# Performance work log

Hardware: AMD Instinct MI355X
Metric: run time of the kernel (lower is better)

## Reference

```python
import jax, jax.numpy as jnp
import numpy as np

N_NODES = 10000
N_EDGES = 160000
MUL0, MUL1 = 32, 8            # multiplicities of 0e and 1o irreps
IN_DIM = MUL0 + 3 * MUL1      # 56
EDGE_FEAT = 64
HIDDEN = 64
# FullyConnectedTensorProduct paths (in x sh -> out):
# (0e,0e)->0e : 32*32=1024 ; (0e,1o)->1o : 32*8=256
# (1o,0e)->1o : 8*8=64     ; (1o,1o)->0e : 8*32=256
W_NUMEL = 1024 + 256 + 64 + 256  # 1600
PATH_NORM = 1.0 / np.sqrt(MUL0 + MUL1)  # 'element' path normalization (fan_in=40)
CG_110 = 1.0 / np.sqrt(3.0)             # normalized w3j for 1x1->0


def setup_inputs() -> dict:
    key = jax.random.key(0)
    ks = jax.random.split(key, 8)
    node_attr = jax.random.normal(ks[0], (N_NODES, IN_DIM), jnp.float32)
    edge_index = jax.random.randint(ks[1], (2, N_EDGES), 0, N_NODES, jnp.int64 if jax.config.read('jax_enable_x64') else jnp.int32)
    edge_attr = jax.random.normal(ks[2], (N_EDGES, EDGE_FEAT), jnp.float32)
    edge_sh = jax.random.normal(ks[3], (N_EDGES, 4), jnp.float32)
    fc_w1 = jax.random.normal(ks[4], (EDGE_FEAT, HIDDEN), jnp.float32) / np.sqrt(EDGE_FEAT)
    fc_b1 = jnp.zeros((HIDDEN,), jnp.float32)
    fc_w2 = jax.random.normal(ks[5], (HIDDEN, W_NUMEL), jnp.float32) / np.sqrt(HIDDEN)
    fc_b2 = jnp.zeros((W_NUMEL,), jnp.float32)
    return {"node_attr": node_attr, "edge_attr": edge_attr, "edge_sh": edge_sh,
            "fc_w1": fc_w1, "fc_b1": fc_b1, "fc_w2": fc_w2, "fc_b2": fc_b2,
            "edge_index": edge_index}


def _tp(x, sh, w):
    # x: [E,56] gathered node feats, sh: [E,4], w: [E,1600] per-edge TP weights
    x0 = x[:, :MUL0]                       # [E,32]   0e scalars
    x1 = x[:, MUL0:].reshape(-1, MUL1, 3)  # [E,8,3]  1o vectors
    sh0 = sh[:, :1]                        # [E,1]
    sh1 = sh[:, 1:4]                       # [E,3]
    w1 = w[:, :1024].reshape(-1, MUL0, MUL0)        # (0e,0e)->0e
    w2 = w[:, 1024:1280].reshape(-1, MUL0, MUL1)    # (0e,1o)->1o
    w3 = w[:, 1280:1344].reshape(-1, MUL1, MUL1)    # (1o,0e)->1o
    w4 = w[:, 1344:1600].reshape(-1, MUL1, MUL0)    # (1o,1o)->0e
    out0 = (jnp.einsum('euv,eu->ev', w1, x0) * sh0
            + CG_110 * jnp.einsum('euv,eum,em->ev', w4, x1, sh1)) * PATH_NORM  # [E,32]
    out1 = (jnp.einsum('euv,eu,em->evm', w2, x0, sh1)
            + jnp.einsum('euv,eum->evm', w3, x1) * sh0[:, :, None]) * PATH_NORM  # [E,8,3]
    return jnp.concatenate([out0, out1.reshape(-1, 3 * MUL1)], axis=-1)  # [E,56]


def reference(node_attr, edge_attr, edge_sh, fc_w1, fc_b1, fc_w2, fc_b2, edge_index):
    edge_src, edge_dst = edge_index[0], edge_index[1]
    # edge MLP -> per-edge tensor-product weights
    h = jax.nn.relu(edge_attr @ fc_w1 + fc_b1)
    w = h @ fc_w2 + fc_b2                                  # [E,1600]
    tp = _tp(node_attr[edge_dst], edge_sh, w)              # gather + TP, [E,56]
    # scatter-mean to source nodes
    n = node_attr.shape[0]
    summed = jax.ops.segment_sum(tp, edge_src, num_segments=n)
    counts = jax.ops.segment_sum(jnp.ones(edge_src.shape, tp.dtype), edge_src, num_segments=n)
    out = summed / jnp.maximum(counts, 1.0)[:, None]
    # residual (pad node_attr up to out width; 0 here since in==out irreps)
    pad = out.shape[-1] - node_attr.shape[-1]
    out = out + jnp.pad(node_attr, ((0, 0), (0, pad)))
    return out
```

## Files before the change

### kernel.cpp

```cpp
#include <hip/hip_runtime.h>

#define NN 10000
#define NE 160000
#define IND 56
#define WN 1600
#define EPB 128
#define NBLK (NE / EPB)
#define DCAP 64

typedef __attribute__((ext_vector_type(8))) short bf16x8;
typedef __attribute__((ext_vector_type(4))) float f32x4;

static constexpr float PATH_NORM_C = 0.15811388300841897f;
static constexpr float CG_C        = 0.57735026918962576f;

__device__ __forceinline__ uint32_t f2bf(float f) {
    uint32_t x = __float_as_uint(f);
    return (x + 0x7fffu + ((x >> 16) & 1u)) >> 16;
}
__device__ __forceinline__ uint32_t pack2(float a, float b) {
    return f2bf(a) | (f2bf(b) << 16);
}
__device__ __forceinline__ f32x4 ld_cf4(const ushort* p) {
    uint2 w = *reinterpret_cast<const uint2*>(p);
    f32x4 v;
    v[0] = __uint_as_float(w.x << 16);
    v[1] = __uint_as_float(w.x & 0xffff0000u);
    v[2] = __uint_as_float(w.y << 16);
    v[3] = __uint_as_float(w.y & 0xffff0000u);
    return v;
}

__global__ __launch_bounds__(256) void prep_kernel(
    const float* __restrict__ fc_w1, const float* __restrict__ fc_w2,
    const int* __restrict__ edge_index,
    ushort* __restrict__ W1T, ushort* __restrict__ W2F,
    int* __restrict__ cursor, int* __restrict__ elist, int do_fill)
{
    int i = blockIdx.x * 256 + threadIdx.x;
    if (i < 64 * 64) {
        int k = i >> 6, j = i & 63;
        W1T[k * 64 + j] = (ushort)f2bf(fc_w1[j * 64 + k]);
    }
    int i2 = i - 64 * 64;
    if (i2 >= 0 && i2 < 100 * 1024) {
        int t  = i2 >> 10, r = i2 & 1023;
        int kh = r >> 9,  rr = r & 511;
        int l  = rr >> 3, ii = rr & 7;
        int j  = t * 16 + (l & 15);
        int k  = kh * 32 + ((l >> 4) << 3) + ii;
        W2F[i2] = (ushort)f2bf(fc_w2[k * WN + j]);
    }
    int i3 = i2 - 100 * 1024;
    if (i3 >= 0 && i3 < NE && do_fill) {
        int s = edge_index[i3];
        int pos = atomicAdd(&cursor[s], 1);
        if (pos < DCAP) elist[s * DCAP + pos] = i3;
    }
}

__global__ __launch_bounds__(256, 3) void edge_kernel(
    const float* __restrict__ node_attr,
    const float* __restrict__ edge_attr,
    const float* __restrict__ edge_sh,
    const float* __restrict__ fc_b1,
    const float* __restrict__ fc_b2,
    const int*   __restrict__ edge_index,
    const ushort* __restrict__ W1T,
    const ushort* __restrict__ W2F,
    float* __restrict__ tpbuf)
{
    __shared__ ushort cfh[64][EPB];
    __shared__ float  shS[4][EPB];
    __shared__ __attribute__((aligned(16))) ushort pool[8192];

    const int tid  = threadIdx.x;
    const int wave = tid >> 6;
    const int lane = tid & 63;
    const int g    = lane >> 4;
    const int q    = lane & 15;
    const int E0   = blockIdx.x * EPB;

    if (tid < EPB) {
        const int e    = tid;
        const int dstn = edge_index[NE + E0 + e];
        const float4 sh = reinterpret_cast<const float4*>(edge_sh)[E0 + e];
        const float4* xp = reinterpret_cast<const float4*>(node_attr + (size_t)dstn * IND);
        float xr[56];
        #pragma unroll
        for (int i = 0; i < 14; ++i) {
            float4 v = xp[i];
            xr[4*i] = v.x; xr[4*i+1] = v.y; xr[4*i+2] = v.z; xr[4*i+3] = v.w;
        }
        #pragma unroll
        for (int u = 0; u < 32; ++u) cfh[u][e] = (ushort)f2bf(xr[u]);
        #pragma unroll
        for (int u = 0; u < 8; ++u) {
            cfh[32 + 3*u + 0][e] = (ushort)f2bf(sh.x * xr[32 + 3*u + 0]);
            cfh[32 + 3*u + 1][e] = (ushort)f2bf(sh.x * xr[32 + 3*u + 1]);
            cfh[32 + 3*u + 2][e] = (ushort)f2bf(sh.x * xr[32 + 3*u + 2]);
            cfh[56 + u][e] = (ushort)f2bf(
                CG_C * (xr[32+3*u]*sh.y + xr[32+3*u+1]*sh.z + xr[32+3*u+2]*sh.w));
        }
        shS[0][e] = sh.x;
        shS[1][e] = sh.y;  shS[2][e] = sh.z;  shS[3][e] = sh.w;
    }

    f32x4 d1[2][4];
    #pragma unroll
    for (int mt = 0; mt < 4; ++mt) {
        const float4 b1v = *reinterpret_cast<const float4*>(fc_b1 + mt*16 + 4*g);
        #pragma unroll
        for (int ms = 0; ms < 2; ++ms)
            d1[ms][mt] = (f32x4){b1v.x, b1v.y, b1v.z, b1v.w};
    }

    #pragma unroll
    for (int kh = 0; kh < 2; ++kh) {
        bf16x8 bfr[2];
        #pragma unroll
        for (int ms = 0; ms < 2; ++ms) {
            const int e = E0 + wave*32 + ms*16 + q;
            const float* ap = edge_attr + (size_t)e * 64 + kh*32 + g*8;
            float4 f0 = *reinterpret_cast<const float4*>(ap);
            float4 f1 = *reinterpret_cast<const float4*>(ap + 4);
            union { uint32_t u[4]; bf16x8 v; } cv;
            cv.u[0] = pack2(f0.x, f0.y); cv.u[1] = pack2(f0.z, f0.w);
            cv.u[2] = pack2(f1.x, f1.y); cv.u[3] = pack2(f1.z, f1.w);
            bfr[ms] = cv.v;
        }
        #pragma unroll
        for (int mt = 0; mt < 4; ++mt) {
            bf16x8 afr = *reinterpret_cast<const bf16x8*>(W1T + (mt*16 + q)*64 + kh*32 + g*8);
            #pragma unroll
            for (int ms = 0; ms < 2; ++ms)
                d1[ms][mt] = __builtin_amdgcn_mfma_f32_16x16x32_bf16(afr, bfr[ms], d1[ms][mt], 0, 0, 0);
        }
    }
    #pragma unroll
    for (int mt = 0; mt < 4; ++mt) {
        const int kg = 2*mt + (g >> 1);
        #pragma unroll
        for (int ms = 0; ms < 2; ++ms) {
            float v0 = fmaxf(d1[ms][mt][0], 0.f);
            float v1 = fmaxf(d1[ms][mt][1], 0.f);
            float v2 = fmaxf(d1[ms][mt][2], 0.f);
            float v3 = fmaxf(d1[ms][mt][3], 0.f);
            uint32_t* wp = reinterpret_cast<uint32_t*>(
                &pool[wave*2048 + ms*1024 + (kg*16 + q)*8 + 4*(g & 1)]);
            wp[0] = pack2(v0, v1);
            wp[1] = pack2(v2, v3);
        }
    }

    bf16x8 af[2][2];
    #pragma unroll
    for (int ms = 0; ms < 2; ++ms)
        #pragma unroll
        for (int kh = 0; kh < 2; ++kh)
            af[ms][kh] = *reinterpret_cast<const bf16x8*>(
                &pool[wave*2048 + ms*1024 + ((kh*4 + g)*16 + q)*8]);

    bf16x8 A0, A1, B0, B1, C0, C1, D0, D1;
    float  Ab, Bb, Cb, Db;
    auto load_slot = [&](int t, bf16x8& b0, bf16x8& b1, float& bb) {
        const ushort* p = W2F + (size_t)t * 1024 + lane * 8;
        b0 = *reinterpret_cast<const bf16x8*>(p);
        b1 = *reinterpret_cast<const bf16x8*>(p + 512);
        bb = fc_b2[t * 16 + q];
    };
    load_slot(0, A0, A1, Ab);
    load_slot(1, B0, B1, Bb);
    load_slot(2, C0, C1, Cb);
    load_slot(3, D0, D1, Db);

    __syncthreads();

    const int ebase = wave*32 + 4*g;
    f32x4 s0v[2];
    s0v[0] = *reinterpret_cast<const f32x4*>(&shS[0][ebase]);
    s0v[1] = *reinterpret_cast<const f32x4*>(&shS[0][ebase + 16]);

    float o0[2][2][4];
    float ttv[2][4];
    float o1v[2][4][3];
    #pragma unroll
    for (int ms = 0; ms < 2; ++ms) {
        #pragma unroll
        for (int r = 0; r < 4; ++r) {
            o0[ms][0][r] = 0.f; o0[ms][1][r] = 0.f; ttv[ms][r] = 0.f;
            o1v[ms][r][0] = 0.f; o1v[ms][r][1] = 0.f; o1v[ms][r][2] = 0.f;
        }
    }

    auto mfma2 = [&](const bf16x8& b0, const bf16x8& b1, float b2v, f32x4* accv) {
        #pragma unroll
        for (int ms = 0; ms < 2; ++ms) {
            f32x4 a = (f32x4){b2v, b2v, b2v, b2v};
            a = __builtin_amdgcn_mfma_f32_16x16x32_bf16(af[ms][0], b0, a, 0, 0, 0);
            a = __builtin_amdgcn_mfma_f32_16x16x32_bf16(af[ms][1], b1, a, 0, 0, 0);
            accv[ms] = a;
        }
    };

    const int qh = q >> 3;

    #pragma unroll 1
    for (int c = 0; c < 16; ++c) {
        const int t4 = 4*c;
        const int u0 = 2*c, u1 = 2*c + 1;
        f32x4 c00 = ld_cf4(&cfh[u0][ebase]);
        f32x4 c01 = ld_cf4(&cfh[u0][ebase + 16]);
        f32x4 c10 = ld_cf4(&cfh[u1][ebase]);
        f32x4 c11 = ld_cf4(&cfh[u1][ebase + 16]);
        f32x4 w2[2];

        mfma2(A0, A1, Ab, w2);  load_slot(t4 + 4, A0, A1, Ab);
        #pragma unroll
        for (int r = 0; r < 4; ++r) {
            o0[0][0][r] = fmaf(s0v[0][r]*c00[r], w2[0][r], o0[0][0][r]);
            o0[1][0][r] = fmaf(s0v[1][r]*c01[r], w2[1][r], o0[1][0][r]);
        }
        mfma2(B0, B1, Bb, w2);  load_slot(t4 + 5, B0, B1, Bb);
        #pragma unroll
        for (int r = 0; r < 4; ++r) {
            o0[0][1][r] = fmaf(s0v[0][r]*c00[r], w2[0][r], o0[0][1][r]);
            o0[1][1][r] = fmaf(s0v[1][r]*c01[r], w2[1][r], o0[1][1][r]);
        }
        mfma2(C0, C1, Cb, w2);  load_slot(t4 + 6, C0, C1, Cb);
        #pragma unroll
        for (int r = 0; r < 4; ++r) {
            o0[0][0][r] = fmaf(s0v[0][r]*c10[r], w2[0][r], o0[0][0][r]);
            o0[1][0][r] = fmaf(s0v[1][r]*c11[r], w2[1][r], o0[1][0][r]);
        }
        mfma2(D0, D1, Db, w2);  load_slot(t4 + 7, D0, D1, Db);
        #pragma unroll
        for (int r = 0; r < 4; ++r) {
            o0[0][1][r] = fmaf(s0v[0][r]*c10[r], w2[0][r], o0[0][1][r]);
            o0[1][1][r] = fmaf(s0v[1][r]*c11[r], w2[1][r], o0[1][1][r]);
        }
    }

    #pragma unroll 1
    for (int d = 0; d < 4; ++d) {
        const int t4 = 64 + 4*d;
        f32x4 w2[2];

        mfma2(A0, A1, Ab, w2);  load_slot(t4 + 4, A0, A1, Ab);
        {
            const int u = 8*d + qh;
            #pragma unroll
            for (int ms = 0; ms < 2; ++ms) {
                f32x4 cfv = ld_cf4(&cfh[u][ebase + ms*16]);
                #pragma unroll
                for (int r = 0; r < 4; ++r) ttv[ms][r] = fmaf(cfv[r], w2[ms][r], ttv[ms][r]);
            }
        }
        mfma2(B0, B1, Bb, w2);  load_slot(t4 + 5, B0, B1, Bb);
        {
            const int u = 8*d + 2 + qh;
            #pragma unroll
            for (int ms = 0; ms < 2; ++ms) {
                f32x4 cfv = ld_cf4(&cfh[u][ebase + ms*16]);
                #pragma unroll
                for (int r = 0; r < 4; ++r) ttv[ms][r] = fmaf(cfv[r], w2[ms][r], ttv[ms][r]);
            }
        }
        mfma2(C0, C1, Cb, w2);  load_slot(t4 + 6, C0, C1, Cb);
        {
            const int u = 8*d + 4 + qh;
            #pragma unroll
            for (int ms = 0; ms < 2; ++ms) {
                f32x4 cfv = ld_cf4(&cfh[u][ebase + ms*16]);
                #pragma unroll
                for (int r = 0; r < 4; ++r) ttv[ms][r] = fmaf(cfv[r], w2[ms][r], ttv[ms][r]);
            }
        }
        mfma2(D0, D1, Db, w2);  load_slot(t4 + 7, D0, D1, Db);
        {
            const int u = 8*d + 6 + qh;
            #pragma unroll
            for (int ms = 0; ms < 2; ++ms) {
                f32x4 cfv = ld_cf4(&cfh[u][ebase + ms*16]);
                #pragma unroll
                for (int r = 0; r < 4; ++r) ttv[ms][r] = fmaf(cfv[r], w2[ms][r], ttv[ms][r]);
            }
        }
    }

    {
        f32x4 w2[2];
        #define R3_BODY(TC)                                                         \
            {                                                                       \
                const int u = 2*(TC) + qh;                                          \
                _Pragma("unroll")                                                   \
                for (int ms = 0; ms < 2; ++ms)                                      \
                    _Pragma("unroll")                                               \
                    for (int m = 0; m < 3; ++m) {                                   \
                        f32x4 cfv = ld_cf4(&cfh[32 + u*3 + m][ebase + ms*16]);      \
                        _Pragma("unroll")                                           \
                        for (int r = 0; r < 4; ++r)                                 \
                            o1v[ms][r][m] = fmaf(cfv[r], w2[ms][r], o1v[ms][r][m]); \
                    }                                                               \
            }
        mfma2(A0, A1, Ab, w2);  load_slot(84, A0, A1, Ab);  R3_BODY(0)
        mfma2(B0, B1, Bb, w2);  load_slot(85, B0, B1, Bb);  R3_BODY(1)
        mfma2(C0, C1, Cb, w2);  load_slot(86, C0, C1, Cb);  R3_BODY(2)
        mfma2(D0, D1, Db, w2);  load_slot(87, D0, D1, Db);  R3_BODY(3)
        #undef R3_BODY
    }

    #pragma unroll 1
    for (int d = 0; d < 4; ++d) {
        const int t4 = 84 + 4*d;
        const int u0 = 2*d, u1 = 2*d + 1;
        f32x4 c00 = ld_cf4(&cfh[56 + u0][ebase]);
        f32x4 c01 = ld_cf4(&cfh[56 + u0][ebase + 16]);
        f32x4 c10 = ld_cf4(&cfh[56 + u1][ebase]);
        f32x4 c11 = ld_cf4(&cfh[56 + u1][ebase + 16]);
        f32x4 w2[2];
        int tn;

        mfma2(A0, A1, Ab, w2);  tn = t4 + 4; load_slot(tn < 100 ? tn : 99, A0, A1, Ab);
        #pragma unroll
        for (int r = 0; r < 4; ++r) {
            o0[0][0][r] = fmaf(c00[r], w2[0][r], o0[0][0][r]);
            o0[1][0][r] = fmaf(c01[r], w2[1][r], o0[1][0][r]);
        }
        mfma2(B0, B1, Bb, w2);  tn = t4 + 5; load_slot(tn < 100 ? tn : 99, B0, B1, Bb);
        #pragma unroll
        for (int r = 0; r < 4; ++r) {
            o0[0][1][r] = fmaf(c00[r], w2[0][r], o0[0][1][r]);
            o0[1][1][r] = fmaf(c01[r], w2[1][r], o0[1][1][r]);
        }
        mfma2(C0, C1, Cb, w2);  tn = t4 + 6; load_slot(tn < 100 ? tn : 99, C0, C1, Cb);
        #pragma unroll
        for (int r = 0; r < 4; ++r) {
            o0[0][0][r] = fmaf(c10[r], w2[0][r], o0[0][0][r]);
            o0[1][0][r] = fmaf(c11[r], w2[1][r], o0[1][0][r]);
        }
        mfma2(D0, D1, Db, w2);  tn = t4 + 7; load_slot(tn < 100 ? tn : 99, D0, D1, Db);
        #pragma unroll
        for (int r = 0; r < 4; ++r) {
            o0[0][1][r] = fmaf(c10[r], w2[0][r], o0[0][1][r]);
            o0[1][1][r] = fmaf(c11[r], w2[1][r], o0[1][1][r]);
        }
    }

    #pragma unroll
    for (int ms = 0; ms < 2; ++ms)
        #pragma unroll
        for (int r = 0; r < 4; ++r) {
            ttv[ms][r] += __shfl_xor(ttv[ms][r], 8, 64);
            #pragma unroll
            for (int m = 0; m < 3; ++m)
                o1v[ms][r][m] += __shfl_xor(o1v[ms][r][m], 8, 64);
        }

    #pragma unroll
    for (int ms = 0; ms < 2; ++ms) {
        const int eb = ebase + ms*16;
        const f32x4 s1x = *reinterpret_cast<const f32x4*>(&shS[1][eb]);
        const f32x4 s1y = *reinterpret_cast<const f32x4*>(&shS[2][eb]);
        const f32x4 s1z = *reinterpret_cast<const f32x4*>(&shS[3][eb]);
        #pragma unroll
        for (int r = 0; r < 4; ++r) {
            float* tp = tpbuf + (size_t)(E0 + eb + r) * IND;
            tp[q]      = PATH_NORM_C * o0[ms][0][r];
            tp[16 + q] = PATH_NORM_C * o0[ms][1][r];
            if ((q & 8) == 0) {
                const int v = q & 7;
                tp[32 + 3*v + 0] = PATH_NORM_C * (o1v[ms][r][0] + s1x[r]*ttv[ms][r]);
                tp[32 + 3*v + 1] = PATH_NORM_C * (o1v[ms][r][1] + s1y[r]*ttv[ms][r]);
                tp[32 + 3*v + 2] = PATH_NORM_C * (o1v[ms][r][2] + s1z[r]*ttv[ms][r]);
            }
        }
    }
}

__global__ __launch_bounds__(256) void gather_kernel(
    const float* __restrict__ tpbuf, const int* __restrict__ cursor,
    const int* __restrict__ elist, const float* __restrict__ node_attr,
    float* __restrict__ out)
{
    const int node = blockIdx.x * 4 + (threadIdx.x >> 6);
    const int j = threadIdx.x & 63;
    if (node >= NN) return;
    const int degt = cursor[node];
    const int deg = (degt < DCAP) ? degt : DCAP;
    float sum = 0.f;
    #pragma unroll 4
    for (int i = 0; i < deg; ++i) {
        const int e = elist[node * DCAP + i];
        if (j < 56) sum += tpbuf[(size_t)e * IND + j];
    }
    if (j < 56) {
        const float c = (degt > 0) ? (float)degt : 1.f;
        out[node * IND + j] = sum / c + node_attr[node * IND + j];
    }
}

__global__ __launch_bounds__(256, 3) void edge_kernel_fb(
    const float* __restrict__ node_attr, const float* __restrict__ edge_attr,
    const float* __restrict__ edge_sh, const float* __restrict__ fc_b1,
    const float* __restrict__ fc_b2, const int* __restrict__ edge_index,
    const ushort* __restrict__ W1T, const ushort* __restrict__ W2F,
    float* __restrict__ acc, float* __restrict__ cnt)
{
    __shared__ ushort cfh[64][EPB];
    __shared__ float  shS[4][EPB];
    __shared__ int    src_lds[EPB];
    __shared__ __attribute__((aligned(16))) ushort pool[8192];

    const int tid  = threadIdx.x;
    const int wave = tid >> 6;
    const int lane = tid & 63;
    const int g    = lane >> 4;
    const int q    = lane & 15;
    const int E0   = blockIdx.x * EPB;

    if (tid < EPB) {
        const int e    = tid;
        const int srcn = edge_index[E0 + e];
        const int dstn = edge_index[NE + E0 + e];
        src_lds[e] = srcn;
        const float4 sh = reinterpret_cast<const float4*>(edge_sh)[E0 + e];
        const float4* xp = reinterpret_cast<const float4*>(node_attr + (size_t)dstn * IND);
        float xr[56];
        #pragma unroll
        for (int i = 0; i < 14; ++i) {
            float4 v = xp[i];
            xr[4*i] = v.x; xr[4*i+1] = v.y; xr[4*i+2] = v.z; xr[4*i+3] = v.w;
        }
        #pragma unroll
        for (int u = 0; u < 32; ++u) cfh[u][e] = (ushort)f2bf(xr[u]);
        #pragma unroll
        for (int u = 0; u < 8; ++u) {
            cfh[32 + 3*u + 0][e] = (ushort)f2bf(sh.x * xr[32 + 3*u + 0]);
            cfh[32 + 3*u + 1][e] = (ushort)f2bf(sh.x * xr[32 + 3*u + 1]);
            cfh[32 + 3*u + 2][e] = (ushort)f2bf(sh.x * xr[32 + 3*u + 2]);
            cfh[56 + u][e] = (ushort)f2bf(
                CG_C * (xr[32+3*u]*sh.y + xr[32+3*u+1]*sh.z + xr[32+3*u+2]*sh.w));
        }
        shS[0][e] = sh.x;
        shS[1][e] = sh.y;  shS[2][e] = sh.z;  shS[3][e] = sh.w;
    }

    f32x4 d1[2][4];
    #pragma unroll
    for (int mt = 0; mt < 4; ++mt) {
        const float4 b1v = *reinterpret_cast<const float4*>(fc_b1 + mt*16 + 4*g);
        #pragma unroll
        for (int ms = 0; ms < 2; ++ms)
            d1[ms][mt] = (f32x4){b1v.x, b1v.y, b1v.z, b1v.w};
    }
    #pragma unroll
    for (int kh = 0; kh < 2; ++kh) {
        bf16x8 bfr[2];
        #pragma unroll
        for (int ms = 0; ms < 2; ++ms) {
            const int e = E0 + wave*32 + ms*16 + q;
            const float* ap = edge_attr + (size_t)e * 64 + kh*32 + g*8;
            float4 f0 = *reinterpret_cast<const float4*>(ap);
            float4 f1 = *reinterpret_cast<const float4*>(ap + 4);
            union { uint32_t u[4]; bf16x8 v; } cv;
            cv.u[0] = pack2(f0.x, f0.y); cv.u[1] = pack2(f0.z, f0.w);
            cv.u[2] = pack2(f1.x, f1.y); cv.u[3] = pack2(f1.z, f1.w);
            bfr[ms] = cv.v;
        }
        #pragma unroll
        for (int mt = 0; mt < 4; ++mt) {
            bf16x8 afr = *reinterpret_cast<const bf16x8*>(W1T + (mt*16 + q)*64 + kh*32 + g*8);
            #pragma unroll
            for (int ms = 0; ms < 2; ++ms)
                d1[ms][mt] = __builtin_amdgcn_mfma_f32_16x16x32_bf16(afr, bfr[ms], d1[ms][mt], 0, 0, 0);
        }
    }
    #pragma unroll
    for (int mt = 0; mt < 4; ++mt) {
        const int kg = 2*mt + (g >> 1);
        #pragma unroll
        for (int ms = 0; ms < 2; ++ms) {
            float v0 = fmaxf(d1[ms][mt][0], 0.f);
            float v1 = fmaxf(d1[ms][mt][1], 0.f);
            float v2 = fmaxf(d1[ms][mt][2], 0.f);
            float v3 = fmaxf(d1[ms][mt][3], 0.f);
            uint32_t* wp = reinterpret_cast<uint32_t*>(
                &pool[wave*2048 + ms*1024 + (kg*16 + q)*8 + 4*(g & 1)]);
            wp[0] = pack2(v0, v1);
            wp[1] = pack2(v2, v3);
        }
    }
    bf16x8 af[2][2];
    #pragma unroll
    for (int ms = 0; ms < 2; ++ms)
        #pragma unroll
        for (int kh = 0; kh < 2; ++kh)
            af[ms][kh] = *reinterpret_cast<const bf16x8*>(
                &pool[wave*2048 + ms*1024 + ((kh*4 + g)*16 + q)*8]);

    bf16x8 A0, A1, B0, B1, C0, C1, D0, D1;
    float  Ab, Bb, Cb, Db;
    auto load_slot = [&](int t, bf16x8& b0, bf16x8& b1, float& bb) {
        const ushort* p = W2F + (size_t)t * 1024 + lane * 8;
        b0 = *reinterpret_cast<const bf16x8*>(p);
        b1 = *reinterpret_cast<const bf16x8*>(p + 512);
        bb = fc_b2[t * 16 + q];
    };
    load_slot(0, A0, A1, Ab);
    load_slot(1, B0, B1, Bb);
    load_slot(2, C0, C1, Cb);
    load_slot(3, D0, D1, Db);
    __syncthreads();

    const int ebase = wave*32 + 4*g;
    f32x4 s0v[2];
    s0v[0] = *reinterpret_cast<const f32x4*>(&shS[0][ebase]);
    s0v[1] = *reinterpret_cast<const f32x4*>(&shS[0][ebase + 16]);
    float o0[2][2][4];
    float ttv[2][4];
    float o1v[2][4][3];
    #pragma unroll
    for (int ms = 0; ms < 2; ++ms)
        #pragma unroll
        for (int r = 0; r < 4; ++r) {
            o0[ms][0][r] = 0.f; o0[ms][1][r] = 0.f; ttv[ms][r] = 0.f;
            o1v[ms][r][0] = 0.f; o1v[ms][r][1] = 0.f; o1v[ms][r][2] = 0.f;
        }
    auto mfma2 = [&](const bf16x8& b0, const bf16x8& b1, float b2v, f32x4* accv) {
        #pragma unroll
        for (int ms = 0; ms < 2; ++ms) {
            f32x4 a = (f32x4){b2v, b2v, b2v, b2v};
            a = __builtin_amdgcn_mfma_f32_16x16x32_bf16(af[ms][0], b0, a, 0, 0, 0);
            a = __builtin_amdgcn_mfma_f32_16x16x32_bf16(af[ms][1], b1, a, 0, 0, 0);
            accv[ms] = a;
        }
    };
    const int qh = q >> 3;
    #pragma unroll 1
    for (int c = 0; c < 16; ++c) {
        const int t4 = 4*c;
        const int u0 = 2*c, u1 = 2*c + 1;
        f32x4 c00 = ld_cf4(&cfh[u0][ebase]);
        f32x4 c01 = ld_cf4(&cfh[u0][ebase + 16]);
        f32x4 c10 = ld_cf4(&cfh[u1][ebase]);
        f32x4 c11 = ld_cf4(&cfh[u1][ebase + 16]);
        f32x4 w2[2];
        mfma2(A0, A1, Ab, w2);  load_slot(t4 + 4, A0, A1, Ab);
        #pragma unroll
        for (int r = 0; r < 4; ++r) {
            o0[0][0][r] = fmaf(s0v[0][r]*c00[r], w2[0][r], o0[0][0][r]);
            o0[1][0][r] = fmaf(s0v[1][r]*c01[r], w2[1][r], o0[1][0][r]);
        }
        mfma2(B0, B1, Bb, w2);  load_slot(t4 + 5, B0, B1, Bb);
        #pragma unroll
        for (int r = 0; r < 4; ++r) {
            o0[0][1][r] = fmaf(s0v[0][r]*c00[r], w2[0][r], o0[0][1][r]);
            o0[1][1][r] = fmaf(s0v[1][r]*c01[r], w2[1][r], o0[1][1][r]);
        }
        mfma2(C0, C1, Cb, w2);  load_slot(t4 + 6, C0, C1, Cb);
        #pragma unroll
        for (int r = 0; r < 4; ++r) {
            o0[0][0][r] = fmaf(s0v[0][r]*c10[r], w2[0][r], o0[0][0][r]);
            o0[1][0][r] = fmaf(s0v[1][r]*c11[r], w2[1][r], o0[1][0][r]);
        }
        mfma2(D0, D1, Db, w2);  load_slot(t4 + 7, D0, D1, Db);
        #pragma unroll
        for (int r = 0; r < 4; ++r) {
            o0[0][1][r] = fmaf(s0v[0][r]*c10[r], w2[0][r], o0[0][1][r]);
            o0[1][1][r] = fmaf(s0v[1][r]*c11[r], w2[1][r], o0[1][1][r]);
        }
    }
    #pragma unroll 1
    for (int d = 0; d < 4; ++d) {
        const int t4 = 64 + 4*d;
        f32x4 w2[2];
        mfma2(A0, A1, Ab, w2);  load_slot(t4 + 4, A0, A1, Ab);
        {
            const int u = 8*d + qh;
            #pragma unroll
            for (int ms = 0; ms < 2; ++ms) {
                f32x4 cfv = ld_cf4(&cfh[u][ebase + ms*16]);
                #pragma unroll
                for (int r = 0; r < 4; ++r) ttv[ms][r] = fmaf(cfv[r], w2[ms][r], ttv[ms][r]);
            }
        }
        mfma2(B0, B1, Bb, w2);  load_slot(t4 + 5, B0, B1, Bb);
        {
            const int u = 8*d + 2 + qh;
            #pragma unroll
            for (int ms = 0; ms < 2; ++ms) {
                f32x4 cfv = ld_cf4(&cfh[u][ebase + ms*16]);
                #pragma unroll
                for (int r = 0; r < 4; ++r) ttv[ms][r] = fmaf(cfv[r], w2[ms][r], ttv[ms][r]);
            }
        }
        mfma2(C0, C1, Cb, w2);  load_slot(t4 + 6, C0, C1, Cb);
        {
            const int u = 8*d + 4 + qh;
            #pragma unroll
            for (int ms = 0; ms < 2; ++ms) {
                f32x4 cfv = ld_cf4(&cfh[u][ebase + ms*16]);
                #pragma unroll
                for (int r = 0; r < 4; ++r) ttv[ms][r] = fmaf(cfv[r], w2[ms][r], ttv[ms][r]);
            }
        }
        mfma2(D0, D1, Db, w2);  load_slot(t4 + 7, D0, D1, Db);
        {
            const int u = 8*d + 6 + qh;
            #pragma unroll
            for (int ms = 0; ms < 2; ++ms) {
                f32x4 cfv = ld_cf4(&cfh[u][ebase + ms*16]);
                #pragma unroll
                for (int r = 0; r < 4; ++r) ttv[ms][r] = fmaf(cfv[r], w2[ms][r], ttv[ms][r]);
            }
        }
    }
    {
        f32x4 w2[2];
        #define R3_BODY(TC)                                                         \
            {                                                                       \
                const int u = 2*(TC) + qh;                                          \
                _Pragma("unroll")                                                   \
                for (int ms = 0; ms < 2; ++ms)                                      \
                    _Pragma("unroll")                                               \
                    for (int m = 0; m < 3; ++m) {                                   \
                        f32x4 cfv = ld_cf4(&cfh[32 + u*3 + m][ebase + ms*16]);      \
                        _Pragma("unroll")                                           \
                        for (int r = 0; r < 4; ++r)                                 \
                            o1v[ms][r][m] = fmaf(cfv[r], w2[ms][r], o1v[ms][r][m]); \
                    }                                                               \
            }
        mfma2(A0, A1, Ab, w2);  load_slot(84, A0, A1, Ab);  R3_BODY(0)
        mfma2(B0, B1, Bb, w2);  load_slot(85, B0, B1, Bb);  R3_BODY(1)
        mfma2(C0, C1, Cb, w2);  load_slot(86, C0, C1, Cb);  R3_BODY(2)
        mfma2(D0, D1, Db, w2);  load_slot(87, D0, D1, Db);  R3_BODY(3)
        #undef R3_BODY
    }
    #pragma unroll 1
    for (int d = 0; d < 4; ++d) {
        const int t4 = 84 + 4*d;
        const int u0 = 2*d, u1 = 2*d + 1;
        f32x4 c00 = ld_cf4(&cfh[56 + u0][ebase]);
        f32x4 c01 = ld_cf4(&cfh[56 + u0][ebase + 16]);
        f32x4 c10 = ld_cf4(&cfh[56 + u1][ebase]);
        f32x4 c11 = ld_cf4(&cfh[56 + u1][ebase + 16]);
        f32x4 w2[2];
        int tn;
        mfma2(A0, A1, Ab, w2);  tn = t4 + 4; load_slot(tn < 100 ? tn : 99, A0, A1, Ab);
        #pragma unroll
        for (int r = 0; r < 4; ++r) {
            o0[0][0][r] = fmaf(c00[r], w2[0][r], o0[0][0][r]);
            o0[1][0][r] = fmaf(c01[r], w2[1][r], o0[1][0][r]);
        }
        mfma2(B0, B1, Bb, w2);  tn = t4 + 5; load_slot(tn < 100 ? tn : 99, B0, B1, Bb);
        #pragma unroll
        for (int r = 0; r < 4; ++r) {
            o0[0][1][r] = fmaf(c00[r], w2[0][r], o0[0][1][r]);
            o0[1][1][r] = fmaf(c01[r], w2[1][r], o0[1][1][r]);
        }
        mfma2(C0, C1, Cb, w2);  tn = t4 + 6; load_slot(tn < 100 ? tn : 99, C0, C1, Cb);
        #pragma unroll
        for (int r = 0; r < 4; ++r) {
            o0[0][0][r] = fmaf(c10[r], w2[0][r], o0[0][0][r]);
            o0[1][0][r] = fmaf(c11[r], w2[1][r], o0[1][0][r]);
        }
        mfma2(D0, D1, Db, w2);  tn = t4 + 7; load_slot(tn < 100 ? tn : 99, D0, D1, Db);
        #pragma unroll
        for (int r = 0; r < 4; ++r) {
            o0[0][1][r] = fmaf(c10[r], w2[0][r], o0[0][1][r]);
            o0[1][1][r] = fmaf(c11[r], w2[1][r], o0[1][1][r]);
        }
    }
    #pragma unroll
    for (int ms = 0; ms < 2; ++ms)
        #pragma unroll
        for (int r = 0; r < 4; ++r) {
            ttv[ms][r] += __shfl_xor(ttv[ms][r], 8, 64);
            #pragma unroll
            for (int m = 0; m < 3; ++m)
                o1v[ms][r][m] += __shfl_xor(o1v[ms][r][m], 8, 64);
        }
    #pragma unroll
    for (int ms = 0; ms < 2; ++ms) {
        const int eb = ebase + ms*16;
        const int4 srcv = *reinterpret_cast<const int4*>(&src_lds[eb]);
        const f32x4 s1x = *reinterpret_cast<const f32x4*>(&shS[1][eb]);
        const f32x4 s1y = *reinterpret_cast<const f32x4*>(&shS[2][eb]);
        const f32x4 s1z = *reinterpret_cast<const f32x4*>(&shS[3][eb]);
        #pragma unroll
        for (int r = 0; r < 4; ++r) {
            const int node = (r == 0) ? srcv.x : (r == 1) ? srcv.y : (r == 2) ? srcv.z : srcv.w;
            float* ap = acc + (size_t)node * IND;
            atomicAdd(ap + q,      PATH_NORM_C * o0[ms][0][r]);
            atomicAdd(ap + 16 + q, PATH_NORM_C * o0[ms][1][r]);
            if ((q & 8) == 0) {
                const int v = q & 7;
                atomicAdd(ap + 32 + 3*v + 0, PATH_NORM_C * (o1v[ms][r][0] + s1x[r]*ttv[ms][r]));
                atomicAdd(ap + 32 + 3*v + 1, PATH_NORM_C * (o1v[ms][r][1] + s1y[r]*ttv[ms][r]));
                atomicAdd(ap + 32 + 3*v + 2, PATH_NORM_C * (o1v[ms][r][2] + s1z[r]*ttv[ms][r]));
            }
        }
    }
    if (lane < 32) atomicAdd(cnt + src_lds[wave*32 + lane], 1.0f);
}

__global__ __launch_bounds__(256) void finalize_kernel(
    const float* __restrict__ acc, const float* __restrict__ cnt,
    const float* __restrict__ node_attr, float* __restrict__ out)
{
    const int i = blockIdx.x * 256 + threadIdx.x;
    if (i >= NN * IND) return;
    const int n = i / IND;
    const float c = fmaxf(cnt[n], 1.0f);
    out[i] = acc[i] / c + node_attr[i];
}

extern "C" void kernel_launch(void* const* d_in, const int* in_sizes, int n_in,
                              void* d_out, int out_size, void* d_ws, size_t ws_size,
                              hipStream_t stream) {
    const float* node_attr = (const float*)d_in[0];
    const float* edge_attr = (const float*)d_in[1];
    const float* edge_sh   = (const float*)d_in[2];
    const float* fc_w1     = (const float*)d_in[3];
    const float* fc_b1     = (const float*)d_in[4];
    const float* fc_w2     = (const float*)d_in[5];
    const float* fc_b2     = (const float*)d_in[6];
    const int*   edge_index = (const int*)d_in[7];

    char* ws = (char*)d_ws;
    int*    cursor = (int*)(ws + 0);
    int*    elist  = (int*)(ws + 40000);
    ushort* W1T    = (ushort*)(ws + 2600000);
    ushort* W2F    = (ushort*)(ws + 2608192);
    float*  tpbuf  = (float*)(ws + 2812992);
    const size_t WS_NEEDED = 2812992ull + (size_t)NE * IND * 4;

    if (ws_size >= WS_NEEDED) {
        hipMemsetAsync(cursor, 0, 40000, stream);
        prep_kernel<<<(64*64 + 100*1024 + NE + 255) / 256, 256, 0, stream>>>(
            fc_w1, fc_w2, edge_index, W1T, W2F, cursor, elist, 1);
        edge_kernel<<<NBLK, 256, 0, stream>>>(
            node_attr, edge_attr, edge_sh, fc_b1, fc_b2, edge_index, W1T, W2F, tpbuf);
        gather_kernel<<<(NN + 3) / 4, 256, 0, stream>>>(
            tpbuf, cursor, elist, node_attr, (float*)d_out);
    } else {
        float*  acc  = (float*)ws;
        float*  cnt  = (float*)(ws + 2240000);
        ushort* W1Tf = (ushort*)(ws + 2280000);
        ushort* W2Ff = (ushort*)(ws + 2288192);
        hipMemsetAsync(ws, 0, 2280000, stream);
        prep_kernel<<<(64*64 + 100*1024 + NE + 255) / 256, 256, 0, stream>>>(
            fc_w1, fc_w2, edge_index, W1Tf, W2Ff, (int*)W1Tf, (int*)W1Tf, 0);
        edge_kernel_fb<<<NBLK, 256, 0, stream>>>(
            node_attr, edge_attr, edge_sh, fc_b1, fc_b2, edge_index, W1Tf, W2Ff, acc, cnt);
        finalize_kernel<<<(NN * IND + 255) / 256, 256, 0, stream>>>(
            acc, cnt, node_attr, (float*)d_out);
    }
}
```

Before: 111.6 us.

## Double edges per block so each wave reuses W2 fragments across 64 edges

Each edge_kernel block now handles 256 edges instead of 128, and each wave handles 64 edges (4 MFMA row tiles instead of 2). Every bf16 W2 fragment loaded from global memory is therefore reused across twice as many edges, halving total W2F traffic, and all 256 threads take part in the node gather. The cost is more accumulator registers and twice the shared memory, so launch bounds drop to 2 blocks per CU and occupancy may fall.

```diff
diff --git a/kernel.cpp b/kernel.cpp
--- a/kernel.cpp
+++ b/kernel.cpp
@@ -6,6 +6,8 @@
 #define WN 1600
 #define EPB 128
 #define NBLK (NE / EPB)
+#define EPB2 256
+#define NBLK2 (NE / EPB2)
 #define DCAP 64
 
 typedef __attribute__((ext_vector_type(8))) short bf16x8;
@@ -59,7 +61,7 @@
     }
 }
 
-__global__ __launch_bounds__(256, 3) void edge_kernel(
+__global__ __launch_bounds__(256, 2) void edge_kernel(
     const float* __restrict__ node_attr,
     const float* __restrict__ edge_attr,
     const float* __restrict__ edge_sh,
@@ -70,18 +72,18 @@
     const ushort* __restrict__ W2F,
     float* __restrict__ tpbuf)
 {
-    __shared__ ushort cfh[64][EPB];
-    __shared__ float  shS[4][EPB];
-    __shared__ __attribute__((aligned(16))) ushort pool[8192];
+    __shared__ ushort cfh[64][EPB2];
+    __shared__ float  shS[4][EPB2];
+    __shared__ __attribute__((aligned(16))) ushort pool[16384];
 
     const int tid  = threadIdx.x;
     const int wave = tid >> 6;
     const int lane = tid & 63;
     const int g    = lane >> 4;
     const int q    = lane & 15;
-    const int E0   = blockIdx.x * EPB;
-
-    if (tid < EPB) {
+    const int E0   = blockIdx.x * EPB2;
+
+    {
         const int e    = tid;
         const int dstn = edge_index[NE + E0 + e];
         const float4 sh = reinterpret_cast<const float4*>(edge_sh)[E0 + e];
@@ -106,21 +108,21 @@
         shS[1][e] = sh.y;  shS[2][e] = sh.z;  shS[3][e] = sh.w;
     }
 
-    f32x4 d1[2][4];
+    f32x4 d1[4][4];
     #pragma unroll
     for (int mt = 0; mt < 4; ++mt) {
         const float4 b1v = *reinterpret_cast<const float4*>(fc_b1 + mt*16 + 4*g);
         #pragma unroll
-        for (int ms = 0; ms < 2; ++ms)
+        for (int ms = 0; ms < 4; ++ms)
             d1[ms][mt] = (f32x4){b1v.x, b1v.y, b1v.z, b1v.w};
     }
 
     #pragma unroll
     for (int kh = 0; kh < 2; ++kh) {
-        bf16x8 bfr[2];
-        #pragma unroll
-        for (int ms = 0; ms < 2; ++ms) {
-            const int e = E0 + wave*32 + ms*16 + q;
+        bf16x8 bfr[4];
+        #pragma unroll
+        for (int ms = 0; ms < 4; ++ms) {
+            const int e = E0 + wave*64 + ms*16 + q;
             const float* ap = edge_attr + (size_t)e * 64 + kh*32 + g*8;
             float4 f0 = *reinterpret_cast<const float4*>(ap);
             float4 f1 = *reinterpret_cast<const float4*>(ap + 4);
@@ -133,7 +135,7 @@
         for (int mt = 0; mt < 4; ++mt) {
             bf16x8 afr = *reinterpret_cast<const bf16x8*>(W1T + (mt*16 + q)*64 + kh*32 + g*8);
             #pragma unroll
-            for (int ms = 0; ms < 2; ++ms)
+            for (int ms = 0; ms < 4; ++ms)
                 d1[ms][mt] = __builtin_amdgcn_mfma_f32_16x16x32_bf16(afr, bfr[ms], d1[ms][mt], 0, 0, 0);
         }
     }
@@ -141,25 +143,25 @@
     for (int mt = 0; mt < 4; ++mt) {
         const int kg = 2*mt + (g >> 1);
         #pragma unroll
-        for (int ms = 0; ms < 2; ++ms) {
+        for (int ms = 0; ms < 4; ++ms) {
             float v0 = fmaxf(d1[ms][mt][0], 0.f);
             float v1 = fmaxf(d1[ms][mt][1], 0.f);
             float v2 = fmaxf(d1[ms][mt][2], 0.f);
             float v3 = fmaxf(d1[ms][mt][3], 0.f);
             uint32_t* wp = reinterpret_cast<uint32_t*>(
-                &pool[wave*2048 + ms*1024 + (kg*16 + q)*8 + 4*(g & 1)]);
+                &pool[wave*4096 + ms*1024 + (kg*16 + q)*8 + 4*(g & 1)]);
             wp[0] = pack2(v0, v1);
             wp[1] = pack2(v2, v3);
         }
     }
 
-    bf16x8 af[2][2];
-    #pragma unroll
-    for (int ms = 0; ms < 2; ++ms)
+    bf16x8 af[4][2];
+    #pragma unroll
+    for (int ms = 0; ms < 4; ++ms)
         #pragma unroll
         for (int kh = 0; kh < 2; ++kh)
             af[ms][kh] = *reinterpret_cast<const bf16x8*>(
-                &pool[wave*2048 + ms*1024 + ((kh*4 + g)*16 + q)*8]);
+                &pool[wave*4096 + ms*1024 + ((kh*4 + g)*16 + q)*8]);
 
     bf16x8 A0, A1, B0, B1, C0, C1, D0, D1;
     float  Ab, Bb, Cb, Db;
@@ -176,16 +178,17 @@
 
     __syncthreads();
 
-    const int ebase = wave*32 + 4*g;
-    f32x4 s0v[2];
-    s0v[0] = *reinterpret_cast<const f32x4*>(&shS[0][ebase]);
-    s0v[1] = *reinterpret_cast<const f32x4*>(&shS[0][ebase + 16]);
-
-    float o0[2][2][4];
-    float ttv[2][4];
-    float o1v[2][4][3];
-    #pragma unroll
-    for (int ms = 0; ms < 2; ++ms) {
+    const int ebase = wave*64 + 4*g;
+    f32x4 s0v[4];
+    #pragma unroll
+    for (int ms = 0; ms < 4; ++ms)
+        s0v[ms] = *reinterpret_cast<const f32x4*>(&shS[0][ebase + ms*16]);
+
+    float o0[4][2][4];
+    float ttv[4][4];
+    float o1v[4][4][3];
+    #pragma unroll
+    for (int ms = 0; ms < 4; ++ms) {
         #pragma unroll
         for (int r = 0; r < 4; ++r) {
             o0[ms][0][r] = 0.f; o0[ms][1][r] = 0.f; ttv[ms][r] = 0.f;
@@ -195,7 +198,7 @@
 
     auto mfma2 = [&](const bf16x8& b0, const bf16x8& b1, float b2v, f32x4* accv) {
         #pragma unroll
-        for (int ms = 0; ms < 2; ++ms) {
+        for (int ms = 0; ms < 4; ++ms) {
             f32x4 a = (f32x4){b2v, b2v, b2v, b2v};
             a = __builtin_amdgcn_mfma_f32_16x16x32_bf16(af[ms][0], b0, a, 0, 0, 0);
             a = __builtin_amdgcn_mfma_f32_16x16x32_bf16(af[ms][1], b1, a, 0, 0, 0);
@@ -208,147 +211,140 @@
     #pragma unroll 1
     for (int c = 0; c < 16; ++c) {
         const int t4 = 4*c;
-        const int u0 = 2*c, u1 = 2*c + 1;
-        f32x4 c00 = ld_cf4(&cfh[u0][ebase]);
-        f32x4 c01 = ld_cf4(&cfh[u0][ebase + 16]);
-        f32x4 c10 = ld_cf4(&cfh[u1][ebase]);
-        f32x4 c11 = ld_cf4(&cfh[u1][ebase + 16]);
-        f32x4 w2[2];
-
-        mfma2(A0, A1, Ab, w2);  load_slot(t4 + 4, A0, A1, Ab);
-        #pragma unroll
-        for (int r = 0; r < 4; ++r) {
-            o0[0][0][r] = fmaf(s0v[0][r]*c00[r], w2[0][r], o0[0][0][r]);
-            o0[1][0][r] = fmaf(s0v[1][r]*c01[r], w2[1][r], o0[1][0][r]);
-        }
-        mfma2(B0, B1, Bb, w2);  load_slot(t4 + 5, B0, B1, Bb);
-        #pragma unroll
-        for (int r = 0; r < 4; ++r) {
-            o0[0][1][r] = fmaf(s0v[0][r]*c00[r], w2[0][r], o0[0][1][r]);
-            o0[1][1][r] = fmaf(s0v[1][r]*c01[r], w2[1][r], o0[1][1][r]);
-        }
-        mfma2(C0, C1, Cb, w2);  load_slot(t4 + 6, C0, C1, Cb);
-        #pragma unroll
-        for (int r = 0; r < 4; ++r) {
-            o0[0][0][r] = fmaf(s0v[0][r]*c10[r], w2[0][r], o0[0][0][r]);
-            o0[1][0][r] = fmaf(s0v[1][r]*c11[r], w2[1][r], o0[1][0][r]);
-        }
-        mfma2(D0, D1, Db, w2);  load_slot(t4 + 7, D0, D1, Db);
-        #pragma unroll
-        for (int r = 0; r < 4; ++r) {
-            o0[0][1][r] = fmaf(s0v[0][r]*c10[r], w2[0][r], o0[0][1][r]);
-            o0[1][1][r] = fmaf(s0v[1][r]*c11[r], w2[1][r], o0[1][1][r]);
-        }
-    }
+        {
+            const int u0 = 2*c;
+            f32x4 cu[4];
+            #pragma unroll
+            for (int ms = 0; ms < 4; ++ms) cu[ms] = ld_cf4(&cfh[u0][ebase + ms*16]);
+            {
+                f32x4 w2[4];
+                mfma2(A0, A1, Ab, w2);  load_slot(t4 + 4, A0, A1, Ab);
+                #pragma unroll
+                for (int ms = 0; ms < 4; ++ms)
+                    #pragma unroll
+                    for (int r = 0; r < 4; ++r)
+                        o0[ms][0][r] = fmaf(s0v[ms][r]*cu[ms][r], w2[ms][r], o0[ms][0][r]);
+            }
+            {
+                f32x4 w2[4];
+                mfma2(B0, B1, Bb, w2);  load_slot(t4 + 5, B0, B1, Bb);
+                #pragma unroll
+                for (int ms = 0; ms < 4; ++ms)
+                    #pragma unroll
+                    for (int r = 0; r < 4; ++r)
+                        o0[ms][1][r] = fmaf(s0v[ms][r]*cu[ms][r], w2[ms][r], o0[ms][1][r]);
+            }
+        }
+        {
+            const int u1 = 2*c + 1;
+            f32x4 cu[4];
+            #pragma unroll
+            for (int ms = 0; ms < 4; ++ms) cu[ms] = ld_cf4(&cfh[u1][ebase + ms*16]);
+            {
+                f32x4 w2[4];
+                mfma2(C0, C1, Cb, w2);  load_slot(t4 + 6, C0, C1, Cb);
+                #pragma unroll
+                for (int ms = 0; ms < 4; ++ms)
+                    #pragma unroll
+                    for (int r = 0; r < 4; ++r)
+                        o0[ms][0][r] = fmaf(s0v[ms][r]*cu[ms][r], w2[ms][r], o0[ms][0][r]);
+            }
+            {
+                f32x4 w2[4];
+                mfma2(D0, D1, Db, w2);  load_slot(t4 + 7, D0, D1, Db);
+                #pragma unroll
+                for (int ms = 0; ms < 4; ++ms)
+                    #pragma unroll
+                    for (int r = 0; r < 4; ++r)
+                        o0[ms][1][r] = fmaf(s0v[ms][r]*cu[ms][r], w2[ms][r], o0[ms][1][r]);
+            }
+        }
+    }
+
+    #define EPI_R2(U) { _Pragma("unroll") for (int ms = 0; ms < 4; ++ms) { \
+        f32x4 cfv = ld_cf4(&cfh[U][ebase + ms*16]); \
+        _Pragma("unroll") for (int r = 0; r < 4; ++r) \
+            ttv[ms][r] = fmaf(cfv[r], w2[ms][r], ttv[ms][r]); } }
 
     #pragma unroll 1
     for (int d = 0; d < 4; ++d) {
         const int t4 = 64 + 4*d;
-        f32x4 w2[2];
-
-        mfma2(A0, A1, Ab, w2);  load_slot(t4 + 4, A0, A1, Ab);
-        {
-            const int u = 8*d + qh;
-            #pragma unroll
-            for (int ms = 0; ms < 2; ++ms) {
-                f32x4 cfv = ld_cf4(&cfh[u][ebase + ms*16]);
-                #pragma unroll
-                for (int r = 0; r < 4; ++r) ttv[ms][r] = fmaf(cfv[r], w2[ms][r], ttv[ms][r]);
-            }
-        }
-        mfma2(B0, B1, Bb, w2);  load_slot(t4 + 5, B0, B1, Bb);
-        {
-            const int u = 8*d + 2 + qh;
-            #pragma unroll
-            for (int ms = 0; ms < 2; ++ms) {
-                f32x4 cfv = ld_cf4(&cfh[u][ebase + ms*16]);
-                #pragma unroll
-                for (int r = 0; r < 4; ++r) ttv[ms][r] = fmaf(cfv[r], w2[ms][r], ttv[ms][r]);
-            }
-        }
-        mfma2(C0, C1, Cb, w2);  load_slot(t4 + 6, C0, C1, Cb);
-        {
-            const int u = 8*d + 4 + qh;
-            #pragma unroll
-            for (int ms = 0; ms < 2; ++ms) {
-                f32x4 cfv = ld_cf4(&cfh[u][ebase + ms*16]);
-                #pragma unroll
-                for (int r = 0; r < 4; ++r) ttv[ms][r] = fmaf(cfv[r], w2[ms][r], ttv[ms][r]);
-            }
-        }
-        mfma2(D0, D1, Db, w2);  load_slot(t4 + 7, D0, D1, Db);
-        {
-            const int u = 8*d + 6 + qh;
-            #pragma unroll
-            for (int ms = 0; ms < 2; ++ms) {
-                f32x4 cfv = ld_cf4(&cfh[u][ebase + ms*16]);
-                #pragma unroll
-                for (int r = 0; r < 4; ++r) ttv[ms][r] = fmaf(cfv[r], w2[ms][r], ttv[ms][r]);
-            }
-        }
-    }
-
+        { f32x4 w2[4]; mfma2(A0, A1, Ab, w2); load_slot(t4 + 4, A0, A1, Ab); EPI_R2(8*d + qh) }
+        { f32x4 w2[4]; mfma2(B0, B1, Bb, w2); load_slot(t4 + 5, B0, B1, Bb); EPI_R2(8*d + 2 + qh) }
+        { f32x4 w2[4]; mfma2(C0, C1, Cb, w2); load_slot(t4 + 6, C0, C1, Cb); EPI_R2(8*d + 4 + qh) }
+        { f32x4 w2[4]; mfma2(D0, D1, Db, w2); load_slot(t4 + 7, D0, D1, Db); EPI_R2(8*d + 6 + qh) }
+    }
+    #undef EPI_R2
+
+    #define EPI_R3(U) { _Pragma("unroll") for (int ms = 0; ms < 4; ++ms) \
+        _Pragma("unroll") for (int m = 0; m < 3; ++m) { \
+            f32x4 cfv = ld_cf4(&cfh[32 + (U)*3 + m][ebase + ms*16]); \
+            _Pragma("unroll") for (int r = 0; r < 4; ++r) \
+                o1v[ms][r][m] = fmaf(cfv[r], w2[ms][r], o1v[ms][r][m]); } }
     {
-        f32x4 w2[2];
-        #define R3_BODY(TC)                                                         \
-            {                                                                       \
-                const int u = 2*(TC) + qh;                                          \
-                _Pragma("unroll")                                                   \
-                for (int ms = 0; ms < 2; ++ms)                                      \
-                    _Pragma("unroll")                                               \
-                    for (int m = 0; m < 3; ++m) {                                   \
-                        f32x4 cfv = ld_cf4(&cfh[32 + u*3 + m][ebase + ms*16]);      \
-                        _Pragma("unroll")                                           \
-                        for (int r = 0; r < 4; ++r)                                 \
-                            o1v[ms][r][m] = fmaf(cfv[r], w2[ms][r], o1v[ms][r][m]); \
-                    }                                                               \
-            }
-        mfma2(A0, A1, Ab, w2);  load_slot(84, A0, A1, Ab);  R3_BODY(0)
-        mfma2(B0, B1, Bb, w2);  load_slot(85, B0, B1, Bb);  R3_BODY(1)
-        mfma2(C0, C1, Cb, w2);  load_slot(86, C0, C1, Cb);  R3_BODY(2)
-        mfma2(D0, D1, Db, w2);  load_slot(87, D0, D1, Db);  R3_BODY(3)
-        #undef R3_BODY
-    }
+        { f32x4 w2[4]; mfma2(A0, A1, Ab, w2); load_slot(84, A0, A1, Ab); EPI_R3(qh) }
+        { f32x4 w2[4]; mfma2(B0, B1, Bb, w2); load_slot(85, B0, B1, Bb); EPI_R3(2 + qh) }
+        { f32x4 w2[4]; mfma2(C0, C1, Cb, w2); load_slot(86, C0, C1, Cb); EPI_R3(4 + qh) }
+        { f32x4 w2[4]; mfma2(D0, D1, Db, w2); load_slot(87, D0, D1, Db); EPI_R3(6 + qh) }
+    }
+    #undef EPI_R3
 
     #pragma unroll 1
     for (int d = 0; d < 4; ++d) {
         const int t4 = 84 + 4*d;
-        const int u0 = 2*d, u1 = 2*d + 1;
-        f32x4 c00 = ld_cf4(&cfh[56 + u0][ebase]);
-        f32x4 c01 = ld_cf4(&cfh[56 + u0][ebase + 16]);
-        f32x4 c10 = ld_cf4(&cfh[56 + u1][ebase]);
-        f32x4 c11 = ld_cf4(&cfh[56 + u1][ebase + 16]);
-        f32x4 w2[2];
         int tn;
-
-        mfma2(A0, A1, Ab, w2);  tn = t4 + 4; load_slot(tn < 100 ? tn : 99, A0, A1, Ab);
-        #pragma unroll
-        for (int r = 0; r < 4; ++r) {
-            o0[0][0][r] = fmaf(c00[r], w2[0][r], o0[0][0][r]);
-            o0[1][0][r] = fmaf(c01[r], w2[1][r], o0[1][0][r]);
-        }
-        mfma2(B0, B1, Bb, w2);  tn = t4 + 5; load_slot(tn < 100 ? tn : 99, B0, B1, Bb);
-        #pragma unroll
-        for (int r = 0; r < 4; ++r) {
-            o0[0][1][r] = fmaf(c00[r], w2[0][r], o0[0][1][r]);
-            o0[1][1][r] = fmaf(c01[r], w2[1][r], o0[1][1][r]);
-        }
-        mfma2(C0, C1, Cb, w2);  tn = t4 + 6; load_slot(tn < 100 ? tn : 99, C0, C1, Cb);
-        #pragma unroll
-        for (int r = 0; r < 4; ++r) {
-            o0[0][0][r] = fmaf(c10[r], w2[0][r], o0[0][0][r]);
-            o0[1][0][r] = fmaf(c11[r], w2[1][r], o0[1][0][r]);
-        }
-        mfma2(D0, D1, Db, w2);  tn = t4 + 7; load_slot(tn < 100 ? tn : 99, D0, D1, Db);
-        #pragma unroll
-        for (int r = 0; r < 4; ++r) {
-            o0[0][1][r] = fmaf(c10[r], w2[0][r], o0[0][1][r]);
-            o0[1][1][r] = fmaf(c11[r], w2[1][r], o0[1][1][r]);
-        }
-    }
-
-    #pragma unroll
-    for (int ms = 0; ms < 2; ++ms)
+        {
+            const int u0 = 2*d;
+            f32x4 cu[4];
+            #pragma unroll
+            for (int ms = 0; ms < 4; ++ms) cu[ms] = ld_cf4(&cfh[56 + u0][ebase + ms*16]);
+            {
+                f32x4 w2[4];
+                mfma2(A0, A1, Ab, w2);  tn = t4 + 4; load_slot(tn < 100 ? tn : 99, A0, A1, Ab);
+                #pragma unroll
+                for (int ms = 0; ms < 4; ++ms)
+                    #pragma unroll
+                    for (int r = 0; r < 4; ++r)
+                        o0[ms][0][r] = fmaf(cu[ms][r], w2[ms][r], o0[ms][0][r]);
+            }
+            {
+                f32x4 w2[4];
+                mfma2(B0, B1, Bb, w2);  tn = t4 + 5; load_slot(tn < 100 ? tn : 99, B0, B1, Bb);
+                #pragma unroll
+                for (int ms = 0; ms < 4; ++ms)
+                    #pragma unroll
+                    for (int r = 0; r < 4; ++r)
+                        o0[ms][1][r] = fmaf(cu[ms][r], w2[ms][r], o0[ms][1][r]);
+            }
+        }
+        {
+            const int u1 = 2*d + 1;
+            f32x4 cu[4];
+            #pragma unroll
+            for (int ms = 0; ms < 4; ++ms) cu[ms] = ld_cf4(&cfh[56 + u1][ebase + ms*16]);
+            {
+                f32x4 w2[4];
+                mfma2(C0, C1, Cb, w2);  tn = t4 + 6; load_slot(tn < 100 ? tn : 99, C0, C1, Cb);
+                #pragma unroll
+                for (int ms = 0; ms < 4; ++ms)
+                    #pragma unroll
+                    for (int r = 0; r < 4; ++r)
+                        o0[ms][0][r] = fmaf(cu[ms][r], w2[ms][r], o0[ms][0][r]);
+            }
+            {
+                f32x4 w2[4];
+                mfma2(D0, D1, Db, w2);  tn = t4 + 7; load_slot(tn < 100 ? tn : 99, D0, D1, Db);
+                #pragma unroll
+                for (int ms = 0; ms < 4; ++ms)
+                    #pragma unroll
+                    for (int r = 0; r < 4; ++r)
+                        o0[ms][1][r] = fmaf(cu[ms][r], w2[ms][r], o0[ms][1][r]);
+            }
+        }
+    }
+
+    #pragma unroll
+    for (int ms = 0; ms < 4; ++ms)
         #pragma unroll
         for (int r = 0; r < 4; ++r) {
             ttv[ms][r] += __shfl_xor(ttv[ms][r], 8, 64);
@@ -358,7 +354,7 @@
         }
 
     #pragma unroll
-    for (int ms = 0; ms < 2; ++ms) {
+    for (int ms = 0; ms < 4; ++ms) {
         const int eb = ebase + ms*16;
         const f32x4 s1x = *reinterpret_cast<const f32x4*>(&shS[1][eb]);
         const f32x4 s1y = *reinterpret_cast<const f32x4*>(&shS[2][eb]);
@@ -740,7 +736,7 @@
         hipMemsetAsync(cursor, 0, 40000, stream);
         prep_kernel<<<(64*64 + 100*1024 + NE + 255) / 256, 256, 0, stream>>>(
             fc_w1, fc_w2, edge_index, W1T, W2F, cursor, elist, 1);
-        edge_kernel<<<NBLK, 256, 0, stream>>>(
+        edge_kernel<<<NBLK2, 256, 0, stream>>>(
             node_attr, edge_attr, edge_sh, fc_b1, fc_b2, edge_index, W1T, W2F, tpbuf);
         gather_kernel<<<(NN + 3) / 4, 256, 0, stream>>>(
             tpbuf, cursor, elist, node_attr, (float*)d_out);
```

After: 123.4 us. 1.11x slower.
